# Kernel optimization log

Measured on AMD Instinct MI355X. Metric: run time of the kernel, lower is better.

The kernel has to match this reference:

```python
import jax, jax.numpy as jnp
import numpy as np

B, L, D = 4, 2048, 1024
H, KD, VD = 16, 64, 64
EPS = 1e-5


def setup_inputs() -> dict:
    key = jax.random.key(0)
    ks = jax.random.split(key, 12)
    s_in = 1.0 / np.sqrt(D)
    s_out = 1.0 / np.sqrt(H * VD)
    return {
        "queries": jax.random.normal(ks[0], (B, L, D), dtype=jnp.float32),
        "Wq": jax.random.uniform(ks[1], (D, H * KD), jnp.float32, -s_in, s_in),
        "bq": jax.random.uniform(ks[2], (H * KD,), jnp.float32, -s_in, s_in),
        "Wk": jax.random.uniform(ks[3], (D, H * KD), jnp.float32, -s_in, s_in),
        "bk": jax.random.uniform(ks[4], (H * KD,), jnp.float32, -s_in, s_in),
        "Wv": jax.random.uniform(ks[5], (D, H * VD), jnp.float32, -s_in, s_in),
        "bv": jax.random.uniform(ks[6], (H * VD,), jnp.float32, -s_in, s_in),
        "Wo": jax.random.uniform(ks[7], (H * VD, D), jnp.float32, -s_out, s_out),
        "bo": jax.random.uniform(ks[8], (D,), jnp.float32, -s_out, s_out),
        "gamma": jnp.ones((D,), jnp.float32),
        "beta": jnp.zeros((D,), jnp.float32),
    }


def reference(queries, Wq, bq, Wk, bk, Wv, bv, Wo, bo, gamma, beta):
    # QKV projections -> [B, L, H, head_dim]
    q = (queries @ Wq + bq).reshape(B, L, H, KD)
    k = (queries @ Wk + bk).reshape(B, L, H, KD)
    v = (queries @ Wv + bv).reshape(B, L, H, VD)
    # scaled dot-product attention per head: scores [B, H, Lq, Lk]
    scores = jnp.einsum("bqhd,bkhd->bhqk", q, k) / np.sqrt(KD).astype(np.float32)
    attn = jax.nn.softmax(scores, axis=-1)
    out = jnp.einsum("bhqk,bkhd->bqhd", attn, v).reshape(B, L, H * VD)
    # out projection (dropout is identity in eval), residual + LayerNorm
    res = out @ Wo + bo + queries
    mu = jnp.mean(res, axis=-1, keepdims=True)
    var = jnp.var(res, axis=-1, keepdims=True)
    return (res - mu) / jnp.sqrt(var + EPS) * gamma + beta
```

## Files before the change

### kernel.cpp

```cpp
#include <hip/hip_runtime.h>
#include <hip/hip_bf16.h>

#define BATCH 4
#define SEQ   2048
#define DIM   1024
#define NHEAD 16
#define HDIM  64
#define EPS_LN 1e-5f
#define QSCALE 0.18033688011112042f

typedef __attribute__((ext_vector_type(8))) short short8;
typedef __attribute__((ext_vector_type(4))) float f32x4;
typedef __attribute__((ext_vector_type(4))) unsigned uint32x4;

__device__ __forceinline__ unsigned short f2bf(float x) {
    __hip_bfloat16 h = __float2bfloat16(x);
    return *reinterpret_cast<unsigned short*>(&h);
}
__device__ __forceinline__ unsigned int pack2bf(float a, float b) {
    __hip_bfloat162 h = __float22bfloat162_rn(float2{a, b});
    return *reinterpret_cast<unsigned int*>(&h);
}

__device__ __forceinline__ void pl32_swap(unsigned& a, unsigned& b) {
    asm("v_permlane32_swap_b32 %0, %1" : "+v"(a), "+v"(b));
}
__device__ __forceinline__ void pl16_swap(unsigned& a, unsigned& b) {
    asm("v_permlane16_swap_b32 %0, %1" : "+v"(a), "+v"(b));
}

__device__ __forceinline__ void gl_lds16(const void* g, void* l) {
    __builtin_amdgcn_global_load_lds(
        (const __attribute__((address_space(1))) unsigned int*)g,
        (__attribute__((address_space(3))) unsigned int*)l,
        16, 0, 0);
}

__global__ __launch_bounds__(256) void prep_kernel(const float* __restrict__ W0,
                                                   const float* __restrict__ W1,
                                                   const float* __restrict__ W2,
                                                   const float* __restrict__ W3,
                                                   const float* __restrict__ queries,
                                                   unsigned short* __restrict__ Wqkvt,
                                                   unsigned short* __restrict__ Wot,
                                                   unsigned short* __restrict__ qout)
{
    const int z = blockIdx.z;
    const int t = threadIdx.x;

    if (z == 4) {
        const int nthr = 16 * 16 * 256;
        int i = (blockIdx.y * 16 + blockIdx.x) * 256 + t;
        for (int it = 0; it < (BATCH * SEQ * DIM / 4) / nthr; it++, i += nthr) {
            float4 v = ((const float4*)queries)[i];
            ushort4 u;
            u.x = f2bf(v.x); u.y = f2bf(v.y); u.z = f2bf(v.z); u.w = f2bf(v.w);
            ((ushort4*)qout)[i] = u;
        }
        return;
    }

    __shared__ float Ts[64][65];
    const float* W = (z == 0) ? W0 : (z == 1) ? W1 : (z == 2) ? W2 : W3;
    unsigned short* Wt = (z == 3) ? Wot : (Wqkvt + (size_t)z * DIM * DIM);

    const int k0 = blockIdx.y * 64, n0 = blockIdx.x * 64;
    const int lr = t >> 2, lq = t & 3;

#pragma unroll
    for (int i = 0; i < 4; i++) {
        float4 v = *(const float4*)(W + (size_t)(k0 + lr) * DIM + n0 + (lq * 4 + i) * 4);
        Ts[lr][(lq * 4 + i) * 4 + 0] = v.x;
        Ts[lr][(lq * 4 + i) * 4 + 1] = v.y;
        Ts[lr][(lq * 4 + i) * 4 + 2] = v.z;
        Ts[lr][(lq * 4 + i) * 4 + 3] = v.w;
    }
    __syncthreads();
#pragma unroll
    for (int i = 0; i < 4; i++) {
        const int c = lq * 16 + i * 4;
        ushort4 u;
        u.x = f2bf(Ts[c + 0][lr]);
        u.y = f2bf(Ts[c + 1][lr]);
        u.z = f2bf(Ts[c + 2][lr]);
        u.w = f2bf(Ts[c + 3][lr]);
        *(ushort4*)(Wt + (size_t)(n0 + lr) * DIM + k0 + c) = u;
    }
}

__global__ __launch_bounds__(256) void gemm_qkv(const unsigned short* __restrict__ A,
                                                const unsigned short* __restrict__ Bt,
                                                const float* __restrict__ bq,
                                                const float* __restrict__ bk,
                                                const float* __restrict__ bv,
                                                unsigned short* __restrict__ Qbf,
                                                unsigned short* __restrict__ Kbf,
                                                unsigned short* __restrict__ Vtb)
{
    __shared__ __attribute__((aligned(16))) unsigned short As[128 * 32];
    __shared__ __attribute__((aligned(16))) unsigned short Bs[128 * 32];

    const int tid = threadIdx.x;
    const int w = tid >> 6, lane = tid & 63;
    const int col = lane & 15, quad = lane >> 4;
    const int wm = (w >> 1) * 64, wn = (w & 1) * 64;
    const int m0 = blockIdx.y * 128, n0 = blockIdx.x * 128;

    f32x4 acc[4][4] = {};
    const int srow = tid >> 2, sc4 = tid & 3;

    for (int k0 = 0; k0 < DIM; k0 += 32) {
        __syncthreads();
#pragma unroll
        for (int it = 0; it < 2; it++) {
            gl_lds16(A  + (size_t)(m0 + srow + it * 64) * DIM + k0 + sc4 * 8,
                     (char*)As + w * 1024 + it * 4096);
            gl_lds16(Bt + (size_t)(n0 + srow + it * 64) * DIM + k0 + sc4 * 8,
                     (char*)Bs + w * 1024 + it * 4096);
        }
        __syncthreads();

        short8 af[4], bf[4];
#pragma unroll
        for (int mt = 0; mt < 4; mt++) af[mt] = *(short8*)&As[(wm + mt * 16 + col) * 32 + quad * 8];
#pragma unroll
        for (int nt = 0; nt < 4; nt++) bf[nt] = *(short8*)&Bs[(wn + nt * 16 + col) * 32 + quad * 8];

#pragma unroll
        for (int mt = 0; mt < 4; mt++)
#pragma unroll
            for (int nt = 0; nt < 4; nt++)
                acc[mt][nt] = __builtin_amdgcn_mfma_f32_16x16x32_bf16(af[mt], bf[nt], acc[mt][nt], 0, 0, 0);
    }

    const int sector = n0 >> 10;
    const float* bias = (sector == 0) ? bq : (sector == 1) ? bk : bv;

#pragma unroll
    for (int nt = 0; nt < 4; nt++) {
        const int n = n0 + wn + nt * 16 + col;
        const int nloc = n - (sector << 10);
        const float bvv = bias[nloc];
#pragma unroll
        for (int mt = 0; mt < 4; mt++) {
            const int mbase = m0 + wm + mt * 16 + quad * 4;
            if (sector == 0) {
#pragma unroll
                for (int r = 0; r < 4; r++)
                    Qbf[(size_t)(mbase + r) * DIM + nloc] = f2bf((acc[mt][nt][r] + bvv) * QSCALE);
            } else if (sector == 1) {
#pragma unroll
                for (int r = 0; r < 4; r++)
                    Kbf[(size_t)(mbase + r) * DIM + nloc] = f2bf(acc[mt][nt][r] + bvv);
            } else {
                const int h = nloc >> 6, d = nloc & 63;
                const int b = mbase >> 11, l = mbase & 2047;
                ushort4 u;
                u.x = f2bf(acc[mt][nt][0] + bvv);
                u.y = f2bf(acc[mt][nt][1] + bvv);
                u.z = f2bf(acc[mt][nt][2] + bvv);
                u.w = f2bf(acc[mt][nt][3] + bvv);
                *(ushort4*)(Vtb + ((size_t)((b * NHEAD + h) * HDIM + d)) * SEQ + l) = u;
            }
        }
    }
}

__global__ __launch_bounds__(256) void gemm_out(const unsigned short* __restrict__ A,
                                                const unsigned short* __restrict__ Bt,
                                                const float* __restrict__ bias,
                                                const float* __restrict__ resid,
                                                float* __restrict__ Cout)
{
    __shared__ __attribute__((aligned(16))) unsigned short As[128 * 32];
    __shared__ __attribute__((aligned(16))) unsigned short Bs[128 * 32];

    const int tid = threadIdx.x;
    const int w = tid >> 6, lane = tid & 63;
    const int col = lane & 15, quad = lane >> 4;
    const int wm = (w >> 1) * 64, wn = (w & 1) * 64;
    const int m0 = blockIdx.y * 128, n0 = blockIdx.x * 128;

    f32x4 acc[4][4] = {};
    const int srow = tid >> 2, sc4 = tid & 3;

    for (int k0 = 0; k0 < DIM; k0 += 32) {
        __syncthreads();
#pragma unroll
        for (int it = 0; it < 2; it++) {
            gl_lds16(A  + (size_t)(m0 + srow + it * 64) * DIM + k0 + sc4 * 8,
                     (char*)As + w * 1024 + it * 4096);
            gl_lds16(Bt + (size_t)(n0 + srow + it * 64) * DIM + k0 + sc4 * 8,
                     (char*)Bs + w * 1024 + it * 4096);
        }
        __syncthreads();

        short8 af[4], bf[4];
#pragma unroll
        for (int mt = 0; mt < 4; mt++) af[mt] = *(short8*)&As[(wm + mt * 16 + col) * 32 + quad * 8];
#pragma unroll
        for (int nt = 0; nt < 4; nt++) bf[nt] = *(short8*)&Bs[(wn + nt * 16 + col) * 32 + quad * 8];

#pragma unroll
        for (int mt = 0; mt < 4; mt++)
#pragma unroll
            for (int nt = 0; nt < 4; nt++)
                acc[mt][nt] = __builtin_amdgcn_mfma_f32_16x16x32_bf16(af[mt], bf[nt], acc[mt][nt], 0, 0, 0);
    }

#pragma unroll
    for (int nt = 0; nt < 4; nt++) {
        const int n = n0 + wn + nt * 16 + col;
        const float bvv = bias[n];
#pragma unroll
        for (int mt = 0; mt < 4; mt++) {
            const int mbase = m0 + wm + mt * 16 + quad * 4;
#pragma unroll
            for (int r = 0; r < 4; r++) {
                const size_t off = (size_t)(mbase + r) * DIM + n;
                Cout[off] = acc[mt][nt][r] + bvv + resid[off];
            }
        }
    }
}

__global__ __launch_bounds__(256) void attn_mfma(const unsigned short* __restrict__ Qb,
                                                 const unsigned short* __restrict__ Kb,
                                                 const unsigned short* __restrict__ Vt,
                                                 unsigned short* __restrict__ Ob)
{
    __shared__ __attribute__((aligned(16))) unsigned short Ks[2 * 64 * 64];
    __shared__ __attribute__((aligned(16))) unsigned short Vs[2 * 64 * 64];

    const int tid = threadIdx.x;
    const int w = tid >> 6, lane = tid & 63;
    const int col = lane & 15, quad = lane >> 4;
    const int cs  = col & 7;
    const int ca  = quad ^ cs;
    const int cb  = (quad ^ 4) ^ cs;

    const int bh  = blockIdx.x & 63;
    const int qt_ = blockIdx.x >> 6;
    const int b   = bh >> 4;
    const int h   = bh & 15;

    const int q0 = qt_ * 128 + w * 32;

    short8 qf[2][2];
#pragma unroll
    for (int qt = 0; qt < 2; qt++) {
        const size_t base = ((size_t)(b * SEQ) + q0 + qt * 16 + col) * DIM + h * HDIM + quad * 8;
        qf[qt][0] = *(const short8*)(Qb + base);
        qf[qt][1] = *(const short8*)(Qb + base + 32);
    }

    short8 onesf;
    {
        const short v = (col == 0) ? (short)0x3F80 : (short)0;
        onesf = short8{v, v, v, v, v, v, v, v};
    }

    f32x4 o[4][2] = {};
    f32x4 od[2]   = {};

    const size_t kbase0 = ((size_t)(b * SEQ)) * DIM + h * HDIM;
    const size_t vbase0 = ((size_t)((b * NHEAD + h) * HDIM)) * SEQ;

    const int lr  = lane >> 3;
    const int swc = (lane & 7) ^ lr;

#pragma unroll
    for (int i = 0; i < 2; i++) {
        const int row = w * 16 + i * 8 + lr;
        gl_lds16(Kb + kbase0 + (size_t)row * DIM + swc * 8,
                 (char*)Ks + w * 2048 + i * 1024);
        gl_lds16(Vt + vbase0 + (size_t)row * SEQ + swc * 8,
                 (char*)Vs + w * 2048 + i * 1024);
    }
    __syncthreads();

    for (int kt = 0; kt < SEQ / 64; kt++) {
        const int cur = kt & 1, nxt = cur ^ 1;
        const unsigned short* Ksb = Ks + cur * 4096;
        const unsigned short* Vsb = Vs + cur * 4096;

        if (kt + 1 < SEQ / 64) {
#pragma unroll
            for (int i = 0; i < 2; i++) {
                const int row = w * 16 + i * 8 + lr;
                gl_lds16(Kb + kbase0 + (size_t)((kt + 1) * 64 + row) * DIM + swc * 8,
                         (char*)Ks + nxt * 8192 + w * 2048 + i * 1024);
                gl_lds16(Vt + vbase0 + (size_t)row * SEQ + (kt + 1) * 64 + swc * 8,
                         (char*)Vs + nxt * 8192 + w * 2048 + i * 1024);
            }
        }

        short8 pf[2][2];
#pragma unroll
        for (int f = 0; f < 2; f++) {
            short8 kfe0 = *(short8*)&Ksb[((f * 2 + 0) * 16 + col) * 64 + ca * 8];
            short8 kfe1 = *(short8*)&Ksb[((f * 2 + 0) * 16 + col) * 64 + cb * 8];
            short8 kfo0 = *(short8*)&Ksb[((f * 2 + 1) * 16 + col) * 64 + ca * 8];
            short8 kfo1 = *(short8*)&Ksb[((f * 2 + 1) * 16 + col) * 64 + cb * 8];
#pragma unroll
            for (int qt = 0; qt < 2; qt++) {
                f32x4 se = {};
                se = __builtin_amdgcn_mfma_f32_16x16x32_bf16(kfe0, qf[qt][0], se, 0, 0, 0);
                se = __builtin_amdgcn_mfma_f32_16x16x32_bf16(kfe1, qf[qt][1], se, 0, 0, 0);
                f32x4 so = {};
                so = __builtin_amdgcn_mfma_f32_16x16x32_bf16(kfo0, qf[qt][0], so, 0, 0, 0);
                so = __builtin_amdgcn_mfma_f32_16x16x32_bf16(kfo1, qf[qt][1], so, 0, 0, 0);

                unsigned a0 = pack2bf(__builtin_amdgcn_exp2f(se[0]), __builtin_amdgcn_exp2f(se[1]));
                unsigned b0 = pack2bf(__builtin_amdgcn_exp2f(se[2]), __builtin_amdgcn_exp2f(se[3]));
                unsigned a1 = pack2bf(__builtin_amdgcn_exp2f(so[0]), __builtin_amdgcn_exp2f(so[1]));
                unsigned b1 = pack2bf(__builtin_amdgcn_exp2f(so[2]), __builtin_amdgcn_exp2f(so[3]));

                pl32_swap(a0, a1);
                pl32_swap(b0, b1);
                pl16_swap(a0, a1);
                pl16_swap(b0, b1);

                uint32x4 cv = {a0, b0, a1, b1};
                pf[qt][f] = __builtin_bit_cast(short8, cv);
            }
        }

        __builtin_amdgcn_s_setprio(1);
#pragma unroll
        for (int qt = 0; qt < 2; qt++) {
            od[qt] = __builtin_amdgcn_mfma_f32_16x16x32_bf16(onesf, pf[qt][0], od[qt], 0, 0, 0);
            od[qt] = __builtin_amdgcn_mfma_f32_16x16x32_bf16(onesf, pf[qt][1], od[qt], 0, 0, 0);
        }

#pragma unroll
        for (int mt = 0; mt < 4; mt++) {
            short8 vf0 = *(short8*)&Vsb[(mt * 16 + col) * 64 + ca * 8];
            short8 vf1 = *(short8*)&Vsb[(mt * 16 + col) * 64 + cb * 8];
#pragma unroll
            for (int qt = 0; qt < 2; qt++) {
                o[mt][qt] = __builtin_amdgcn_mfma_f32_16x16x32_bf16(vf0, pf[qt][0], o[mt][qt], 0, 0, 0);
                o[mt][qt] = __builtin_amdgcn_mfma_f32_16x16x32_bf16(vf1, pf[qt][1], o[mt][qt], 0, 0, 0);
            }
        }
        __builtin_amdgcn_s_setprio(0);

        __syncthreads();
    }

#pragma unroll
    for (int qt = 0; qt < 2; qt++) {
        const float den = __shfl(od[qt][0], col);
        const float inv = 1.f / den;
        const size_t rowoff = ((size_t)(b * SEQ) + q0 + qt * 16 + col) * DIM + h * HDIM;
#pragma unroll
        for (int mt = 0; mt < 4; mt++) {
            ushort4 u;
            u.x = f2bf(o[mt][qt][0] * inv);
            u.y = f2bf(o[mt][qt][1] * inv);
            u.z = f2bf(o[mt][qt][2] * inv);
            u.w = f2bf(o[mt][qt][3] * inv);
            *(ushort4*)(Ob + rowoff + mt * 16 + quad * 4) = u;
        }
    }
}

__global__ __launch_bounds__(256) void layernorm_kernel(float* __restrict__ res,
                                                        const float* __restrict__ gamma,
                                                        const float* __restrict__ beta)
{
    const int tid = threadIdx.x;
    const int row = blockIdx.x;
    float4 xv = ((const float4*)(res + (size_t)row * DIM))[tid];

    float s  = xv.x + xv.y + xv.z + xv.w;
    float sq = xv.x * xv.x + xv.y * xv.y + xv.z * xv.z + xv.w * xv.w;
#pragma unroll
    for (int off = 32; off; off >>= 1) {
        s  += __shfl_xor(s, off);
        sq += __shfl_xor(sq, off);
    }
    __shared__ float sm[8];
    const int w = tid >> 6, lane = tid & 63;
    if (lane == 0) { sm[w] = s; sm[4 + w] = sq; }
    __syncthreads();
    const float st  = sm[0] + sm[1] + sm[2] + sm[3];
    const float sqt = sm[4] + sm[5] + sm[6] + sm[7];
    const float mu   = st * (1.f / DIM);
    const float var  = sqt * (1.f / DIM) - mu * mu;
    const float rstd = rsqrtf(var + EPS_LN);

    float4 g  = ((const float4*)gamma)[tid];
    float4 be = ((const float4*)beta)[tid];
    float4 o;
    o.x = (xv.x - mu) * rstd * g.x + be.x;
    o.y = (xv.y - mu) * rstd * g.y + be.y;
    o.z = (xv.z - mu) * rstd * g.z + be.z;
    o.w = (xv.w - mu) * rstd * g.w + be.w;
    ((float4*)(res + (size_t)row * DIM))[tid] = o;
}

extern "C" void kernel_launch(void* const* d_in, const int* in_sizes, int n_in,
                              void* d_out, int out_size, void* d_ws, size_t ws_size,
                              hipStream_t stream)
{
    const float* queries = (const float*)d_in[0];
    const float* Wq = (const float*)d_in[1];
    const float* bq = (const float*)d_in[2];
    const float* Wk = (const float*)d_in[3];
    const float* bk = (const float*)d_in[4];
    const float* Wv = (const float*)d_in[5];
    const float* bv = (const float*)d_in[6];
    const float* Wo = (const float*)d_in[7];
    const float* bo = (const float*)d_in[8];
    const float* gamma = (const float*)d_in[9];
    const float* beta  = (const float*)d_in[10];
    float* outp = (float*)d_out;

    const int M = BATCH * SEQ;
    const size_t BUF = (size_t)M * DIM;
    const size_t WSZ = (size_t)DIM * DIM;

    unsigned short* w0  = (unsigned short*)d_ws;
    unsigned short* qin = w0;
    unsigned short* Qbf = w0 + BUF;
    unsigned short* Kbf = w0 + 2 * BUF;
    unsigned short* Vtb = w0 + 3 * BUF;
    unsigned short* Wqkvt = w0 + 4 * BUF;
    unsigned short* Wot   = Wqkvt + 3 * WSZ;
    unsigned short* Obf = qin;

    dim3 blk(256);

    dim3 pgrid(DIM / 64, DIM / 64, 5);
    prep_kernel<<<pgrid, blk, 0, stream>>>(Wq, Wk, Wv, Wo, queries, Wqkvt, Wot, qin);

    dim3 qkvgrid(3 * DIM / 128, M / 128);
    gemm_qkv<<<qkvgrid, blk, 0, stream>>>(qin, Wqkvt, bq, bk, bv, Qbf, Kbf, Vtb);

    attn_mfma<<<BATCH * NHEAD * (SEQ / 128), blk, 0, stream>>>(Qbf, Kbf, Vtb, Obf);

    dim3 ogrid(DIM / 128, M / 128);
    gemm_out<<<ogrid, blk, 0, stream>>>(Obf, Wot, bo, queries, outp);

    layernorm_kernel<<<M, blk, 0, stream>>>(outp, gamma, beta);
}
```

Before: 322.5 us.

## Split attention block into 8 waves of 16 query rows each

The attention kernel now runs 512 threads per block, so each of the 8 waves handles 16 query rows instead of 32, and each wave loads one 8-row slice of the K/V tile instead of two. Per-wave registers for Q fragments and output accumulators are halved, which should raise occupancy and spread the cooperative K/V loads across more waves. In exchange, every K fragment read from LDS now feeds only one query tile, so LDS traffic per MFMA doubles and more waves contend at each barrier.

```diff
diff --git a/kernel.cpp b/kernel.cpp
--- a/kernel.cpp
+++ b/kernel.cpp
@@ -224,7 +224,7 @@
     }
 }
 
-__global__ __launch_bounds__(256) void attn_mfma(const unsigned short* __restrict__ Qb,
+__global__ __launch_bounds__(512) void attn_mfma(const unsigned short* __restrict__ Qb,
                                                  const unsigned short* __restrict__ Kb,
                                                  const unsigned short* __restrict__ Vt,
                                                  unsigned short* __restrict__ Ob)
@@ -244,14 +244,13 @@
     const int b   = bh >> 4;
     const int h   = bh & 15;
 
-    const int q0 = qt_ * 128 + w * 32;
-
-    short8 qf[2][2];
-#pragma unroll
-    for (int qt = 0; qt < 2; qt++) {
-        const size_t base = ((size_t)(b * SEQ) + q0 + qt * 16 + col) * DIM + h * HDIM + quad * 8;
-        qf[qt][0] = *(const short8*)(Qb + base);
-        qf[qt][1] = *(const short8*)(Qb + base + 32);
+    const int q0 = qt_ * 128 + w * 16;
+
+    short8 qf0, qf1;
+    {
+        const size_t base = ((size_t)(b * SEQ) + q0 + col) * DIM + h * HDIM + quad * 8;
+        qf0 = *(const short8*)(Qb + base);
+        qf1 = *(const short8*)(Qb + base + 32);
     }
 
     short8 onesf;
@@ -260,8 +259,8 @@
         onesf = short8{v, v, v, v, v, v, v, v};
     }
 
-    f32x4 o[4][2] = {};
-    f32x4 od[2]   = {};
+    f32x4 o[4] = {};
+    f32x4 od   = {};
 
     const size_t kbase0 = ((size_t)(b * SEQ)) * DIM + h * HDIM;
     const size_t vbase0 = ((size_t)((b * NHEAD + h) * HDIM)) * SEQ;
@@ -269,13 +268,10 @@
     const int lr  = lane >> 3;
     const int swc = (lane & 7) ^ lr;
 
-#pragma unroll
-    for (int i = 0; i < 2; i++) {
-        const int row = w * 16 + i * 8 + lr;
-        gl_lds16(Kb + kbase0 + (size_t)row * DIM + swc * 8,
-                 (char*)Ks + w * 2048 + i * 1024);
-        gl_lds16(Vt + vbase0 + (size_t)row * SEQ + swc * 8,
-                 (char*)Vs + w * 2048 + i * 1024);
+    {
+        const int row = w * 8 + lr;
+        gl_lds16(Kb + kbase0 + (size_t)row * DIM + swc * 8, (char*)Ks + w * 1024);
+        gl_lds16(Vt + vbase0 + (size_t)row * SEQ + swc * 8, (char*)Vs + w * 1024);
     }
     __syncthreads();
 
@@ -285,81 +281,69 @@
         const unsigned short* Vsb = Vs + cur * 4096;
 
         if (kt + 1 < SEQ / 64) {
-#pragma unroll
-            for (int i = 0; i < 2; i++) {
-                const int row = w * 16 + i * 8 + lr;
-                gl_lds16(Kb + kbase0 + (size_t)((kt + 1) * 64 + row) * DIM + swc * 8,
-                         (char*)Ks + nxt * 8192 + w * 2048 + i * 1024);
-                gl_lds16(Vt + vbase0 + (size_t)row * SEQ + (kt + 1) * 64 + swc * 8,
-                         (char*)Vs + nxt * 8192 + w * 2048 + i * 1024);
-            }
-        }
-
-        short8 pf[2][2];
+            const int row = w * 8 + lr;
+            gl_lds16(Kb + kbase0 + (size_t)((kt + 1) * 64 + row) * DIM + swc * 8,
+                     (char*)Ks + nxt * 8192 + w * 1024);
+            gl_lds16(Vt + vbase0 + (size_t)row * SEQ + (kt + 1) * 64 + swc * 8,
+                     (char*)Vs + nxt * 8192 + w * 1024);
+        }
+
+        short8 pf[2];
 #pragma unroll
         for (int f = 0; f < 2; f++) {
             short8 kfe0 = *(short8*)&Ksb[((f * 2 + 0) * 16 + col) * 64 + ca * 8];
             short8 kfe1 = *(short8*)&Ksb[((f * 2 + 0) * 16 + col) * 64 + cb * 8];
             short8 kfo0 = *(short8*)&Ksb[((f * 2 + 1) * 16 + col) * 64 + ca * 8];
             short8 kfo1 = *(short8*)&Ksb[((f * 2 + 1) * 16 + col) * 64 + cb * 8];
-#pragma unroll
-            for (int qt = 0; qt < 2; qt++) {
-                f32x4 se = {};
-                se = __builtin_amdgcn_mfma_f32_16x16x32_bf16(kfe0, qf[qt][0], se, 0, 0, 0);
-                se = __builtin_amdgcn_mfma_f32_16x16x32_bf16(kfe1, qf[qt][1], se, 0, 0, 0);
-                f32x4 so = {};
-                so = __builtin_amdgcn_mfma_f32_16x16x32_bf16(kfo0, qf[qt][0], so, 0, 0, 0);
-                so = __builtin_amdgcn_mfma_f32_16x16x32_bf16(kfo1, qf[qt][1], so, 0, 0, 0);
-
-                unsigned a0 = pack2bf(__builtin_amdgcn_exp2f(se[0]), __builtin_amdgcn_exp2f(se[1]));
-                unsigned b0 = pack2bf(__builtin_amdgcn_exp2f(se[2]), __builtin_amdgcn_exp2f(se[3]));
-                unsigned a1 = pack2bf(__builtin_amdgcn_exp2f(so[0]), __builtin_amdgcn_exp2f(so[1]));
-                unsigned b1 = pack2bf(__builtin_amdgcn_exp2f(so[2]), __builtin_amdgcn_exp2f(so[3]));
-
-                pl32_swap(a0, a1);
-                pl32_swap(b0, b1);
-                pl16_swap(a0, a1);
-                pl16_swap(b0, b1);
-
-                uint32x4 cv = {a0, b0, a1, b1};
-                pf[qt][f] = __builtin_bit_cast(short8, cv);
-            }
+
+            f32x4 se = {};
+            se = __builtin_amdgcn_mfma_f32_16x16x32_bf16(kfe0, qf0, se, 0, 0, 0);
+            se = __builtin_amdgcn_mfma_f32_16x16x32_bf16(kfe1, qf1, se, 0, 0, 0);
+            f32x4 so = {};
+            so = __builtin_amdgcn_mfma_f32_16x16x32_bf16(kfo0, qf0, so, 0, 0, 0);
+            so = __builtin_amdgcn_mfma_f32_16x16x32_bf16(kfo1, qf1, so, 0, 0, 0);
+
+            unsigned a0 = pack2bf(__builtin_amdgcn_exp2f(se[0]), __builtin_amdgcn_exp2f(se[1]));
+            unsigned b0 = pack2bf(__builtin_amdgcn_exp2f(se[2]), __builtin_amdgcn_exp2f(se[3]));
+            unsigned a1 = pack2bf(__builtin_amdgcn_exp2f(so[0]), __builtin_amdgcn_exp2f(so[1]));
+            unsigned b1 = pack2bf(__builtin_amdgcn_exp2f(so[2]), __builtin_amdgcn_exp2f(so[3]));
+
+            pl32_swap(a0, a1);
+            pl32_swap(b0, b1);
+            pl16_swap(a0, a1);
+            pl16_swap(b0, b1);
+
+            uint32x4 cv = {a0, b0, a1, b1};
+            pf[f] = __builtin_bit_cast(short8, cv);
         }
 
         __builtin_amdgcn_s_setprio(1);
-#pragma unroll
-        for (int qt = 0; qt < 2; qt++) {
-            od[qt] = __builtin_amdgcn_mfma_f32_16x16x32_bf16(onesf, pf[qt][0], od[qt], 0, 0, 0);
-            od[qt] = __builtin_amdgcn_mfma_f32_16x16x32_bf16(onesf, pf[qt][1], od[qt], 0, 0, 0);
-        }
+        od = __builtin_amdgcn_mfma_f32_16x16x32_bf16(onesf, pf[0], od, 0, 0, 0);
+        od = __builtin_amdgcn_mfma_f32_16x16x32_bf16(onesf, pf[1], od, 0, 0, 0);
 
 #pragma unroll
         for (int mt = 0; mt < 4; mt++) {
             short8 vf0 = *(short8*)&Vsb[(mt * 16 + col) * 64 + ca * 8];
             short8 vf1 = *(short8*)&Vsb[(mt * 16 + col) * 64 + cb * 8];
-#pragma unroll
-            for (int qt = 0; qt < 2; qt++) {
-                o[mt][qt] = __builtin_amdgcn_mfma_f32_16x16x32_bf16(vf0, pf[qt][0], o[mt][qt], 0, 0, 0);
-                o[mt][qt] = __builtin_amdgcn_mfma_f32_16x16x32_bf16(vf1, pf[qt][1], o[mt][qt], 0, 0, 0);
-            }
+            o[mt] = __builtin_amdgcn_mfma_f32_16x16x32_bf16(vf0, pf[0], o[mt], 0, 0, 0);
+            o[mt] = __builtin_amdgcn_mfma_f32_16x16x32_bf16(vf1, pf[1], o[mt], 0, 0, 0);
         }
         __builtin_amdgcn_s_setprio(0);
 
         __syncthreads();
     }
 
-#pragma unroll
-    for (int qt = 0; qt < 2; qt++) {
-        const float den = __shfl(od[qt][0], col);
+    {
+        const float den = __shfl(od[0], col);
         const float inv = 1.f / den;
-        const size_t rowoff = ((size_t)(b * SEQ) + q0 + qt * 16 + col) * DIM + h * HDIM;
+        const size_t rowoff = ((size_t)(b * SEQ) + q0 + col) * DIM + h * HDIM;
 #pragma unroll
         for (int mt = 0; mt < 4; mt++) {
             ushort4 u;
-            u.x = f2bf(o[mt][qt][0] * inv);
-            u.y = f2bf(o[mt][qt][1] * inv);
-            u.z = f2bf(o[mt][qt][2] * inv);
-            u.w = f2bf(o[mt][qt][3] * inv);
+            u.x = f2bf(o[mt][0] * inv);
+            u.y = f2bf(o[mt][1] * inv);
+            u.z = f2bf(o[mt][2] * inv);
+            u.w = f2bf(o[mt][3] * inv);
             *(ushort4*)(Ob + rowoff + mt * 16 + quad * 4) = u;
         }
     }
@@ -438,7 +422,7 @@
     dim3 qkvgrid(3 * DIM / 128, M / 128);
     gemm_qkv<<<qkvgrid, blk, 0, stream>>>(qin, Wqkvt, bq, bk, bv, Qbf, Kbf, Vtb);
 
-    attn_mfma<<<BATCH * NHEAD * (SEQ / 128), blk, 0, stream>>>(Qbf, Kbf, Vtb, Obf);
+    attn_mfma<<<BATCH * NHEAD * (SEQ / 128), dim3(512), 0, stream>>>(Qbf, Kbf, Vtb, Obf);
 
     dim3 ogrid(DIM / 128, M / 128);
     gemm_out<<<ogrid, blk, 0, stream>>>(Obf, Wot, bo, queries, outp);
```

Result: faster. 308.5 us (-4.3%).

## Switch attention MFMAs to 32x32x16 tiles and compute softmax denominator on VALU

Applied to the files above, without the earlier changes.

Rewrites the attention inner loop to use 32x32x16 bf16 MFMA instructions instead of 16x16x32, so each wave covers 32 query rows with a single tile. The register and LDS fragment layouts are reworked to match, and only permlane32 swaps are needed to turn the score accumulator into a P operand. The softmax denominator is now summed in fp32 on the VALU and reduced across half-waves at the end, replacing the extra ones-vector MFMAs. This cuts MFMA instruction count and permute overhead, but puts more accumulator registers and VALU adds in the loop.

```diff
diff --git a/kernel.cpp b/kernel.cpp
--- a/kernel.cpp
+++ b/kernel.cpp
@@ -11,6 +11,7 @@
 
 typedef __attribute__((ext_vector_type(8))) short short8;
 typedef __attribute__((ext_vector_type(4))) float f32x4;
+typedef __attribute__((ext_vector_type(16))) float f32x16;
 typedef __attribute__((ext_vector_type(4))) unsigned uint32x4;
 
 __device__ __forceinline__ unsigned short f2bf(float x) {
@@ -24,9 +25,6 @@
 
 __device__ __forceinline__ void pl32_swap(unsigned& a, unsigned& b) {
     asm("v_permlane32_swap_b32 %0, %1" : "+v"(a), "+v"(b));
-}
-__device__ __forceinline__ void pl16_swap(unsigned& a, unsigned& b) {
-    asm("v_permlane16_swap_b32 %0, %1" : "+v"(a), "+v"(b));
 }
 
 __device__ __forceinline__ void gl_lds16(const void* g, void* l) {
@@ -234,10 +232,8 @@
 
     const int tid = threadIdx.x;
     const int w = tid >> 6, lane = tid & 63;
-    const int col = lane & 15, quad = lane >> 4;
-    const int cs  = col & 7;
-    const int ca  = quad ^ cs;
-    const int cb  = (quad ^ 4) ^ cs;
+    const int l31 = lane & 31, hi = lane >> 5;
+    const int sw7 = l31 & 7;
 
     const int bh  = blockIdx.x & 63;
     const int qt_ = blockIdx.x >> 6;
@@ -246,22 +242,13 @@
 
     const int q0 = qt_ * 128 + w * 32;
 
-    short8 qf[2][2];
-#pragma unroll
-    for (int qt = 0; qt < 2; qt++) {
-        const size_t base = ((size_t)(b * SEQ) + q0 + qt * 16 + col) * DIM + h * HDIM + quad * 8;
-        qf[qt][0] = *(const short8*)(Qb + base);
-        qf[qt][1] = *(const short8*)(Qb + base + 32);
-    }
-
-    short8 onesf;
-    {
-        const short v = (col == 0) ? (short)0x3F80 : (short)0;
-        onesf = short8{v, v, v, v, v, v, v, v};
-    }
-
-    f32x4 o[4][2] = {};
-    f32x4 od[2]   = {};
+    short8 qf[4];
+#pragma unroll
+    for (int ds = 0; ds < 4; ds++)
+        qf[ds] = *(const short8*)(Qb + ((size_t)(b * SEQ) + q0 + l31) * DIM + h * HDIM + ds * 16 + hi * 8);
+
+    f32x16 o[2] = {};
+    float dsum = 0.f;
 
     const size_t kbase0 = ((size_t)(b * SEQ)) * DIM + h * HDIM;
     const size_t vbase0 = ((size_t)((b * NHEAD + h) * HDIM)) * SEQ;
@@ -272,10 +259,8 @@
 #pragma unroll
     for (int i = 0; i < 2; i++) {
         const int row = w * 16 + i * 8 + lr;
-        gl_lds16(Kb + kbase0 + (size_t)row * DIM + swc * 8,
-                 (char*)Ks + w * 2048 + i * 1024);
-        gl_lds16(Vt + vbase0 + (size_t)row * SEQ + swc * 8,
-                 (char*)Vs + w * 2048 + i * 1024);
+        gl_lds16(Kb + kbase0 + (size_t)row * DIM + swc * 8, (char*)Ks + w * 2048 + i * 1024);
+        gl_lds16(Vt + vbase0 + (size_t)row * SEQ + swc * 8, (char*)Vs + w * 2048 + i * 1024);
     }
     __syncthreads();
 
@@ -297,72 +282,69 @@
 
         short8 pf[2][2];
 #pragma unroll
-        for (int f = 0; f < 2; f++) {
-            short8 kfe0 = *(short8*)&Ksb[((f * 2 + 0) * 16 + col) * 64 + ca * 8];
-            short8 kfe1 = *(short8*)&Ksb[((f * 2 + 0) * 16 + col) * 64 + cb * 8];
-            short8 kfo0 = *(short8*)&Ksb[((f * 2 + 1) * 16 + col) * 64 + ca * 8];
-            short8 kfo1 = *(short8*)&Ksb[((f * 2 + 1) * 16 + col) * 64 + cb * 8];
-#pragma unroll
-            for (int qt = 0; qt < 2; qt++) {
-                f32x4 se = {};
-                se = __builtin_amdgcn_mfma_f32_16x16x32_bf16(kfe0, qf[qt][0], se, 0, 0, 0);
-                se = __builtin_amdgcn_mfma_f32_16x16x32_bf16(kfe1, qf[qt][1], se, 0, 0, 0);
-                f32x4 so = {};
-                so = __builtin_amdgcn_mfma_f32_16x16x32_bf16(kfo0, qf[qt][0], so, 0, 0, 0);
-                so = __builtin_amdgcn_mfma_f32_16x16x32_bf16(kfo1, qf[qt][1], so, 0, 0, 0);
-
-                unsigned a0 = pack2bf(__builtin_amdgcn_exp2f(se[0]), __builtin_amdgcn_exp2f(se[1]));
-                unsigned b0 = pack2bf(__builtin_amdgcn_exp2f(se[2]), __builtin_amdgcn_exp2f(se[3]));
-                unsigned a1 = pack2bf(__builtin_amdgcn_exp2f(so[0]), __builtin_amdgcn_exp2f(so[1]));
-                unsigned b1 = pack2bf(__builtin_amdgcn_exp2f(so[2]), __builtin_amdgcn_exp2f(so[3]));
-
-                pl32_swap(a0, a1);
-                pl32_swap(b0, b1);
-                pl16_swap(a0, a1);
-                pl16_swap(b0, b1);
-
-                uint32x4 cv = {a0, b0, a1, b1};
-                pf[qt][f] = __builtin_bit_cast(short8, cv);
+        for (int kb = 0; kb < 2; kb++) {
+            f32x16 s = {};
+#pragma unroll
+            for (int ds = 0; ds < 4; ds++) {
+                short8 kf = *(const short8*)&Ksb[(kb * 32 + l31) * 64 + (((ds * 2 + hi) ^ sw7) * 8)];
+                s = __builtin_amdgcn_mfma_f32_32x32x16_bf16(kf, qf[ds], s, 0, 0, 0);
             }
+            unsigned d0, d1, d2, d3, d4, d5, d6, d7;
+            {
+                float p0, p1;
+                p0 = __builtin_amdgcn_exp2f(s[0]);  p1 = __builtin_amdgcn_exp2f(s[1]);
+                dsum += p0 + p1;  d0 = pack2bf(p0, p1);
+                p0 = __builtin_amdgcn_exp2f(s[2]);  p1 = __builtin_amdgcn_exp2f(s[3]);
+                dsum += p0 + p1;  d1 = pack2bf(p0, p1);
+                p0 = __builtin_amdgcn_exp2f(s[4]);  p1 = __builtin_amdgcn_exp2f(s[5]);
+                dsum += p0 + p1;  d2 = pack2bf(p0, p1);
+                p0 = __builtin_amdgcn_exp2f(s[6]);  p1 = __builtin_amdgcn_exp2f(s[7]);
+                dsum += p0 + p1;  d3 = pack2bf(p0, p1);
+                p0 = __builtin_amdgcn_exp2f(s[8]);  p1 = __builtin_amdgcn_exp2f(s[9]);
+                dsum += p0 + p1;  d4 = pack2bf(p0, p1);
+                p0 = __builtin_amdgcn_exp2f(s[10]); p1 = __builtin_amdgcn_exp2f(s[11]);
+                dsum += p0 + p1;  d5 = pack2bf(p0, p1);
+                p0 = __builtin_amdgcn_exp2f(s[12]); p1 = __builtin_amdgcn_exp2f(s[13]);
+                dsum += p0 + p1;  d6 = pack2bf(p0, p1);
+                p0 = __builtin_amdgcn_exp2f(s[14]); p1 = __builtin_amdgcn_exp2f(s[15]);
+                dsum += p0 + p1;  d7 = pack2bf(p0, p1);
+            }
+            pl32_swap(d0, d2);  pl32_swap(d1, d3);
+            pl32_swap(d4, d6);  pl32_swap(d5, d7);
+            pf[kb][0] = __builtin_bit_cast(short8, uint32x4{d0, d1, d2, d3});
+            pf[kb][1] = __builtin_bit_cast(short8, uint32x4{d4, d5, d6, d7});
         }
 
         __builtin_amdgcn_s_setprio(1);
 #pragma unroll
-        for (int qt = 0; qt < 2; qt++) {
-            od[qt] = __builtin_amdgcn_mfma_f32_16x16x32_bf16(onesf, pf[qt][0], od[qt], 0, 0, 0);
-            od[qt] = __builtin_amdgcn_mfma_f32_16x16x32_bf16(onesf, pf[qt][1], od[qt], 0, 0, 0);
-        }
-
-#pragma unroll
-        for (int mt = 0; mt < 4; mt++) {
-            short8 vf0 = *(short8*)&Vsb[(mt * 16 + col) * 64 + ca * 8];
-            short8 vf1 = *(short8*)&Vsb[(mt * 16 + col) * 64 + cb * 8];
-#pragma unroll
-            for (int qt = 0; qt < 2; qt++) {
-                o[mt][qt] = __builtin_amdgcn_mfma_f32_16x16x32_bf16(vf0, pf[qt][0], o[mt][qt], 0, 0, 0);
-                o[mt][qt] = __builtin_amdgcn_mfma_f32_16x16x32_bf16(vf1, pf[qt][1], o[mt][qt], 0, 0, 0);
-            }
-        }
+        for (int db = 0; db < 2; db++)
+#pragma unroll
+            for (int kb = 0; kb < 2; kb++)
+#pragma unroll
+                for (int ks = 0; ks < 2; ks++) {
+                    short8 vf = *(const short8*)&Vsb[(db * 32 + l31) * 64 + (((kb * 4 + ks * 2 + hi) ^ sw7) * 8)];
+                    o[db] = __builtin_amdgcn_mfma_f32_32x32x16_bf16(vf, pf[kb][ks], o[db], 0, 0, 0);
+                }
         __builtin_amdgcn_s_setprio(0);
 
         __syncthreads();
     }
 
-#pragma unroll
-    for (int qt = 0; qt < 2; qt++) {
-        const float den = __shfl(od[qt][0], col);
-        const float inv = 1.f / den;
-        const size_t rowoff = ((size_t)(b * SEQ) + q0 + qt * 16 + col) * DIM + h * HDIM;
-#pragma unroll
-        for (int mt = 0; mt < 4; mt++) {
+    const float den = dsum + __shfl_xor(dsum, 32);
+    const float inv = 1.f / den;
+
+    const size_t rowoff = ((size_t)(b * SEQ) + q0 + l31) * DIM + h * HDIM;
+#pragma unroll
+    for (int db = 0; db < 2; db++)
+#pragma unroll
+        for (int g = 0; g < 4; g++) {
             ushort4 u;
-            u.x = f2bf(o[mt][qt][0] * inv);
-            u.y = f2bf(o[mt][qt][1] * inv);
-            u.z = f2bf(o[mt][qt][2] * inv);
-            u.w = f2bf(o[mt][qt][3] * inv);
-            *(ushort4*)(Ob + rowoff + mt * 16 + quad * 4) = u;
-        }
-    }
+            u.x = f2bf(o[db][g * 4 + 0] * inv);
+            u.y = f2bf(o[db][g * 4 + 1] * inv);
+            u.z = f2bf(o[db][g * 4 + 2] * inv);
+            u.w = f2bf(o[db][g * 4 + 3] * inv);
+            *(ushort4*)(Ob + rowoff + db * 32 + g * 8 + hi * 4) = u;
+        }
 }
 
 __global__ __launch_bounds__(256) void layernorm_kernel(float* __restrict__ res,
```

Measured after the change: 318.8 us. Within noise of the previous version (-1.1%).
